# Kernel optimization log

Measured on AMD Instinct MI355X. Metric: run time of the kernel, lower is better.

## Reference

```python
import jax, jax.numpy as jnp
import numpy as np

S, T, B = 128, 64, 64          # src_len, trg_len, batch
E, H, D, A, V = 512, 512, 1024, 256, 32000  # emb, enc_hid, dec_hid(=2H), attn, vocab
PAD = 0


def _p(key, shape, scale=0.02):
    return jax.random.normal(key, shape, dtype=jnp.float32) * scale


def setup_inputs() -> dict:
    key = jax.random.key(0)
    ks = jax.random.split(key, 20)
    return {
        'src': jax.random.randint(ks[0], (S, B), 0, V, dtype=jnp.int32),
        'trg': jax.random.randint(ks[1], (T, B), 0, V, dtype=jnp.int32),
        'enc_emb': _p(ks[2], (V, E)),
        'Wf_ih': _p(ks[3], (4 * H, E)), 'Wf_hh': _p(ks[4], (4 * H, H)), 'bf': jnp.zeros((4 * H,), jnp.float32),
        'Wb_ih': _p(ks[5], (4 * H, E)), 'Wb_hh': _p(ks[6], (4 * H, H)), 'bb': jnp.zeros((4 * H,), jnp.float32),
        'Wa': _p(ks[7], (A, 2 * H + D)), 'ba': jnp.zeros((A,), jnp.float32),
        'v': _p(ks[8], (A,)),
        'dec_emb': _p(ks[9], (V, E)),
        'Wd_ih': _p(ks[10], (4 * D, E + 2 * H)), 'Wd_hh': _p(ks[11], (4 * D, D)), 'bd': jnp.zeros((4 * D,), jnp.float32),
        'Wo': _p(ks[12], (V, 2 * H + D + E)), 'bo': jnp.zeros((V,), jnp.float32),
    }


def lstm_cell(x, h, c, W_ih, W_hh, b):
    # PyTorch gate order: i, f, g, o
    g = x @ W_ih.T + h @ W_hh.T + b
    i, f, gg, o = jnp.split(g, 4, axis=-1)
    c2 = jax.nn.sigmoid(f) * c + jax.nn.sigmoid(i) * jnp.tanh(gg)
    h2 = jax.nn.sigmoid(o) * jnp.tanh(c2)
    return h2, c2


def seq2seq_fwd(src, trg, enc_emb, Wf_ih, Wf_hh, bf, Wb_ih, Wb_hh, bb,
                Wa, ba, v, dec_emb, Wd_ih, Wd_hh, bd, Wo, bo):
    emb = enc_emb[src]                                   # [S,B,E]
    z = jnp.zeros((B, H), emb.dtype)

    def fstep(carry, x):
        h, c = lstm_cell(x, *carry, Wf_ih, Wf_hh, bf)
        return (h, c), h

    def bstep(carry, x):
        h, c = lstm_cell(x, *carry, Wb_ih, Wb_hh, bb)
        return (h, c), h

    (hf, cf), hs_f = jax.lax.scan(fstep, (z, z), emb)
    (hb, cb), hs_b = jax.lax.scan(bstep, (z, z), emb[::-1])
    enc_out = jnp.concatenate([hs_f, hs_b[::-1]], axis=-1)   # [S,B,2H]

    h0 = jnp.concatenate([hf, hb], axis=-1)              # [B,D]
    c0 = jnp.concatenate([cf, cb], axis=-1)

    mask = (src != PAD).T                                # [B,S]
    enc_bse = enc_out.transpose(1, 0, 2)                 # [B,S,2H]

    def dstep(carry, tok):
        h, c = carry
        emb_t = dec_emb[tok]                             # [B,E]
        hrep = jnp.broadcast_to(h[:, None, :], (B, S, D))
        energy = jnp.tanh(jnp.concatenate([hrep, enc_bse], -1) @ Wa.T + ba)  # [B,S,A]
        scores = energy @ v                              # [B,S]
        scores = jnp.where(mask, scores, jnp.float32(-1e10))
        a = jax.nn.softmax(scores, axis=1)
        ctx = jnp.einsum('bs,bse->be', a, enc_bse)       # [B,2H]
        x = jnp.concatenate([emb_t, ctx], axis=-1)
        h2, c2 = lstm_cell(x, h, c, Wd_ih, Wd_hh, bd)
        pred = jnp.concatenate([h2, ctx, emb_t], -1) @ Wo.T + bo  # [B,V]
        return (h2, c2), pred

    # teacher_forcing_ratio = 1.0 -> input at step t is trg[t-1]
    _, preds = jax.lax.scan(dstep, (h0, c0), trg[:-1])
    outputs = jnp.concatenate([jnp.zeros((1, B, V), preds.dtype), preds], axis=0)
    return outputs                                       # [T,B,V]


def reference(src, trg, enc_emb, Wf_ih, Wf_hh, bf, Wb_ih, Wb_hh, bb,
              Wa, ba, v, dec_emb, Wd_ih, Wd_hh, bd, Wo, bo):
    return seq2seq_fwd(src, trg, enc_emb, Wf_ih, Wf_hh, bf, Wb_ih, Wb_hh, bb,
                       Wa, ba, v, dec_emb, Wd_ih, Wd_hh, bd, Wo, bo)
```

## Files before the change

kernel.cpp:

```cpp
#include <hip/hip_runtime.h>

#define SLEN  128
#define BATCH 64
#define EMB   512
#define HID   512
#define DDEC  1024
#define ATT   256
#define VOC   32000
#define TSTEPS 63
#define SLOT  1024

typedef _Float16 f16x4 __attribute__((ext_vector_type(4)));
typedef _Float16 f16x8 __attribute__((ext_vector_type(8)));
typedef float    f32x4 __attribute__((ext_vector_type(4)));

union HQ  { unsigned long long q[2]; f16x8 v; };
union HP  { _Float16 h[2]; unsigned u; };
union HP4 { _Float16 h[4]; f16x4 v4; unsigned long long u; };

__device__ __forceinline__ float sigmoidf_(float x) { return 1.0f / (1.0f + __expf(-x)); }
__device__ __forceinline__ float tanhf_(float x)    { return 1.0f - 2.0f / (__expf(2.0f * x) + 1.0f); }

__device__ __forceinline__ void st_u32(void* p, unsigned v) {
    __hip_atomic_store((unsigned*)p, v, __ATOMIC_RELAXED, __HIP_MEMORY_SCOPE_AGENT);
}
__device__ __forceinline__ void st_u64(void* p, unsigned long long v) {
    __hip_atomic_store((unsigned long long*)p, v, __ATOMIC_RELAXED, __HIP_MEMORY_SCOPE_AGENT);
}
__device__ __forceinline__ unsigned long long ld_u64(const void* p) {
    return __hip_atomic_load((const unsigned long long*)p, __ATOMIC_RELAXED, __HIP_MEMORY_SCOPE_AGENT);
}
__device__ __forceinline__ void st_i32(int* p, int v) {
    __hip_atomic_store(p, v, __ATOMIC_RELAXED, __HIP_MEMORY_SCOPE_AGENT);
}
__device__ __forceinline__ int ld_i32(const int* p) {
    return __hip_atomic_load(p, __ATOMIC_RELAXED, __HIP_MEMORY_SCOPE_AGENT);
}

__device__ __forceinline__ void bar_arrive(int* flags, int myid, int epoch) {
    __syncthreads();
    if (threadIdx.x == 0) st_i32(flags + myid * SLOT, epoch);
}
__device__ __forceinline__ void bar_wait(int* flags, int nf, int epoch) {
    if ((int)threadIdx.x < 64) {
        bool done = false;
        while (!done) {
            bool ok = true;
            for (int i = threadIdx.x; i < nf; i += 64)
                ok = ok && (ld_i32(flags + i * SLOT) >= epoch);
            done = __all(ok);
            if (!done) __builtin_amdgcn_s_sleep(1);
        }
    }
    __syncthreads();
}

__global__ __launch_bounds__(256) void init_convert(
    const int* __restrict__ src, const int* __restrict__ trg,
    const float* __restrict__ enc_emb, const float* __restrict__ dec_emb,
    const float* __restrict__ Wf_ih, const float* __restrict__ Wf_hh,
    const float* __restrict__ Wb_ih, const float* __restrict__ Wb_hh,
    const float* __restrict__ Wa, const float* __restrict__ Wd_ih, const float* __restrict__ Wd_hh,
    float* __restrict__ out0,
    _Float16* __restrict__ Wenc16, _Float16* __restrict__ Wd16, _Float16* __restrict__ Wa16,
    _Float16* __restrict__ emb_src16, _Float16* __restrict__ predA,
    float* __restrict__ c_enc, _Float16* __restrict__ h16_enc, int* __restrict__ bar_ws)
{
    long idx = (long)blockIdx.x * 256 + threadIdx.x;
    if (idx < 2048000L) { out0[idx] = 0.f; return; }
    idx -= 2048000L;
    if (idx < 4194304L) {
        int dir = (int)(idx >> 21);
        int rem = (int)(idx & ((1 << 21) - 1));
        int rr = rem >> 10, c = rem & 1023;
        int d = rr >> 2, qg = rr & 3;
        const float* Wih = dir ? Wb_ih : Wf_ih;
        const float* Whh = dir ? Wb_hh : Wf_hh;
        float v = (c < 512) ? Wih[(long)(qg * 512 + d) * 512 + c]
                            : Whh[(long)(qg * 512 + d) * 512 + (c - 512)];
        Wenc16[idx] = (_Float16)v; return;
    }
    idx -= 4194304L;
    if (idx < 10485760L) {
        int rr = (int)(idx / 2560), c = (int)(idx % 2560);
        int d = rr >> 2, qg = rr & 3;
        float v = (c < 1536) ? Wd_ih[(long)(qg * 1024 + d) * 1536 + c]
                             : Wd_hh[(long)(qg * 1024 + d) * 1024 + (c - 1536)];
        Wd16[idx] = (_Float16)v; return;
    }
    idx -= 10485760L;
    if (idx < 262144L) {
        int rr = (int)(idx >> 10), c = (int)(idx & 1023);
        Wa16[idx] = (_Float16)Wa[(long)rr * 2048 + c]; return;
    }
    idx -= 262144L;
    if (idx < 4194304L) {
        int sb = (int)(idx >> 9), e = (int)(idx & 511);
        int tok = src[sb];
        emb_src16[idx] = (_Float16)enc_emb[(long)tok * 512 + e]; return;
    }
    idx -= 4194304L;
    if (idx < 2064384L) {
        int rI = (int)(idx >> 9), e = (int)(idx & 511);
        int tok = trg[rI];
        predA[(long)(64 + rI) * 2560 + 2048 + e] = (_Float16)dec_emb[(long)tok * 512 + e]; return;
    }
    idx -= 2064384L;
    if (idx < 65536L) { c_enc[idx] = 0.f; return; }
    idx -= 65536L;
    if (idx < 65536L) { h16_enc[idx] = (_Float16)0.f; return; }
    idx -= 65536L;
    if (idx < 655360L) { bar_ws[idx] = 0; }
}

__global__ __launch_bounds__(256, 1) void enc_coop(
    const _Float16* __restrict__ Wenc16, const _Float16* __restrict__ emb_src16,
    _Float16* __restrict__ h16_enc, float* __restrict__ c_enc,
    const float* __restrict__ bf, const float* __restrict__ bb,
    _Float16* __restrict__ enc_out16, int* __restrict__ bar_ws)
{
    __shared__ _Float16 Wl[32768];
    __shared__ float gbuf[32][34];

    const int t = threadIdx.x, lane = t & 63, wv = t >> 6;
    const int blk = blockIdx.x;
    const int g = blk >> 6, wb = blk & 63;
    const int dir = g >> 1, bh = g & 1;
    const int r16 = lane & 15, kg = lane >> 4;
    int* eflags = bar_ws + (384 + g * 64) * SLOT;

    #pragma unroll
    for (int i = 0; i < 16; ++i) {
        int h0 = (i * 256 + t) * 8;
        int kc = h0 >> 10;
        int rem = h0 & 1023;
        int gt2 = rem >> 9, l = (rem >> 3) & 63;
        f16x8 v = *(const f16x8*)(Wenc16 +
            ((size_t)(dir * 2048 + wb * 32 + gt2 * 16 + (l & 15))) * 1024 + (l >> 4) * 8 + kc * 32);
        *(f16x8*)&Wl[h0] = v;
    }

    const float* bias = dir ? bb : bf;
    const int pb = t & 31, dp = t >> 5;
    const int dl0 = dp * 2;
    float bias2[2][4], creg2[2] = {0.f, 0.f};
    if (t < 128) {
        #pragma unroll
        for (int j = 0; j < 2; ++j)
            #pragma unroll
            for (int q = 0; q < 4; ++q)
                bias2[j][q] = bias[q * 512 + wb * 8 + dl0 + j];
    }
    __syncthreads();

    for (int s = 0; s < SLEN; ++s) {
        const int par = s & 1;
        const int s_eff = dir ? (127 - s) : s;
        const int gt = wv & 1, mb = wv >> 1;
        const int arow = bh * 32 + mb * 16 + r16;
        const _Float16* Ax = emb_src16 + ((size_t)(s_eff * 64 + arow)) * 512 + kg * 8;
        const unsigned long long* Hq =
            (const unsigned long long*)(h16_enc + ((size_t)((par * 2 + dir) * 64 + arow)) * 512);
        f32x4 acc = {};
        #pragma unroll 4
        for (int kc = 0; kc < 16; ++kc) {
            f16x8 bw = *(const f16x8*)&Wl[kc * 1024 + gt * 512 + lane * 8];
            f16x8 a  = *(const f16x8*)(Ax + kc * 32);
            acc = __builtin_amdgcn_mfma_f32_16x16x32_f16(a, bw, acc, 0, 0, 0);
        }
        #pragma unroll 4
        for (int kc = 0; kc < 16; ++kc) {
            f16x8 bw = *(const f16x8*)&Wl[(16 + kc) * 1024 + gt * 512 + lane * 8];
            HQ hq;
            hq.q[0] = ld_u64(Hq + kc * 8 + kg * 2);
            hq.q[1] = ld_u64(Hq + kc * 8 + kg * 2 + 1);
            acc = __builtin_amdgcn_mfma_f32_16x16x32_f16(hq.v, bw, acc, 0, 0, 0);
        }
        #pragma unroll
        for (int rI = 0; rI < 4; ++rI)
            gbuf[gt * 16 + (lane & 15)][mb * 16 + kg * 4 + rI] = acc[rI];
        __syncthreads();
        if (t < 128) {
            HP hp;
            #pragma unroll
            for (int j = 0; j < 2; ++j) {
                const int dl = dl0 + j;
                float g0 = gbuf[dl * 4 + 0][pb] + bias2[j][0];
                float g1 = gbuf[dl * 4 + 1][pb] + bias2[j][1];
                float g2 = gbuf[dl * 4 + 2][pb] + bias2[j][2];
                float g3 = gbuf[dl * 4 + 3][pb] + bias2[j][3];
                float c2 = sigmoidf_(g1) * creg2[j] + sigmoidf_(g0) * tanhf_(g2);
                float h2 = sigmoidf_(g3) * tanhf_(c2);
                creg2[j] = c2;
                hp.h[j] = (_Float16)h2;
            }
            const int bglob = bh * 32 + pb;
            const int d0 = wb * 8 + dl0;
            st_u32((void*)(h16_enc + ((size_t)((par ^ 1) * 2 + dir) * 64 + bglob) * 512 + d0), hp.u);
            *(unsigned*)(enc_out16 + ((size_t)s_eff * 64 + bglob) * 1024 + dir * 512 + d0) = hp.u;
        }
        bar_arrive(eflags, wb, s + 1);
        bar_wait(eflags, 64, s + 1);
    }
    if (t < 128) {
        const int bglob = bh * 32 + pb;
        const int d0 = wb * 8 + dl0;
        c_enc[((size_t)dir * 64 + bglob) * 512 + d0] = creg2[0];
        c_enc[((size_t)dir * 64 + bglob) * 512 + d0 + 1] = creg2[1];
    }
}

__global__ __launch_bounds__(256, 1) void dec_coop(
    const _Float16* __restrict__ Wd16, const _Float16* __restrict__ Wa16,
    const float* __restrict__ bd, const float* __restrict__ vvec,
    const int* __restrict__ src, const _Float16* __restrict__ enc_part16,
    const _Float16* __restrict__ enc_out16, const float* __restrict__ c_enc,
    _Float16* __restrict__ predA, int* __restrict__ bar_ws)
{
    __shared__ _Float16 Wl[40960];
    __shared__ float gbuf[16][68];
    __shared__ float ha[256], sv[256], sc[128], esum[256], red[4];

    const int t = threadIdx.x, lane = t & 63, wv = t >> 6;
    const int r16 = lane & 15, kg = lane >> 4;
    const int blk = blockIdx.x;
    const int gid = blk;
    int* cf  = bar_ws;
    int* hs  = bar_ws + 64 * SLOT;
    int* hf0 = bar_ws + 320 * SLOT;

    #pragma unroll
    for (int i = 0; i < 20; ++i) {
        int h0 = (i * 256 + t) * 8;
        int kc = h0 >> 9, l = (h0 >> 3) & 63;
        f16x8 v = *(const f16x8*)(Wd16 + ((size_t)(gid * 16 + (l & 15))) * 2560 + (l >> 4) * 8 + kc * 32);
        *(f16x8*)&Wl[h0] = v;
    }

    const int pb = t & 63;
    const int dl0 = (t >> 6) * 2;
    float bias2[2][4], creg2[2] = {0.f, 0.f};
    if (t < 128) {
        #pragma unroll
        for (int j = 0; j < 2; ++j) {
            const int dg = gid * 4 + dl0 + j;
            #pragma unroll
            for (int q = 0; q < 4; ++q) bias2[j][q] = bd[q * 1024 + dg];
            creg2[j] = (dg < 512) ? c_enc[(size_t)pb * 512 + dg]
                                  : c_enc[(size_t)(64 + pb) * 512 + (dg - 512)];
        }
    }

    if (blk < 64) {
        sv[t] = vvec[t];
        {
            const int d0 = t * 4;
            const size_t rbase = (d0 < 512) ? (size_t)(127 * 64 + blk) * 1024
                                            : (size_t)(0 * 64 + blk) * 1024;
            HP4 o;
            o.h[0] = enc_out16[rbase + d0];
            o.h[1] = enc_out16[rbase + d0 + 1];
            o.h[2] = enc_out16[rbase + d0 + 2];
            o.h[3] = enc_out16[rbase + d0 + 3];
            st_u64((void*)(predA + (size_t)blk * 2560 + d0), o.u);
        }
        bar_arrive(hf0, blk, 1);
    } else {
        __syncthreads();
    }

    for (int tt = 0; tt < TSTEPS; ++tt) {
        if (tt == 0) bar_wait(hf0, 64, 1); else bar_wait(hs, 256, tt);

        if (blk < 64) {
            const int wb = blk;
            {
                const int base_m = wb & 48;
                const _Float16* Ahh = predA + ((size_t)(tt * 64 + base_m + r16)) * 2560 + kg * 8;
                f32x4 acc4[4] = {};
                #pragma unroll 4
                for (int kc = 0; kc < 32; ++kc) {
                    f16x8 a = *(const f16x8*)(Ahh + kc * 32);
                    #pragma unroll
                    for (int jj = 0; jj < 4; ++jj) {
                        f16x8 bw = *(const f16x8*)(Wa16 +
                            ((size_t)((wv * 4 + jj) * 16 + r16)) * 1024 + kg * 8 + kc * 32);
                        acc4[jj] = __builtin_amdgcn_mfma_f32_16x16x32_f16(a, bw, acc4[jj], 0, 0, 0);
                    }
                }
                if (kg == ((wb & 15) >> 2)) {
                    #pragma unroll
                    for (int jj = 0; jj < 4; ++jj)
                        ha[(wv * 4 + jj) * 16 + r16] = acc4[jj][wb & 3];
                }
            }
            __syncthreads();
            {
                const int s = t & 127, jh = t >> 7;
                const f16x8* ep = (const f16x8*)(enc_part16 + ((size_t)s * 64 + wb) * 256 + jh * 128);
                float acc = 0.f;
                #pragma unroll 2
                for (int j8 = 0; j8 < 16; ++j8) {
                    f16x8 e = ep[j8];
                    #pragma unroll
                    for (int u = 0; u < 8; ++u)
                        acc += tanhf_(ha[jh * 128 + j8 * 8 + u] + (float)e[u]) * sv[jh * 128 + j8 * 8 + u];
                }
                esum[t] = acc;
            }
            __syncthreads();
            if (t < 128) {
                float scv = esum[t] + esum[128 + t];
                scv = (src[t * 64 + wb] != 0) ? scv : -1e10f;
                sc[t] = scv;
                float v = scv;
                #pragma unroll
                for (int off = 32; off > 0; off >>= 1) v = fmaxf(v, __shfl_xor(v, off));
                if (lane == 0) red[t >> 6] = v;
            }
            __syncthreads();
            {
                const float mx = fmaxf(red[0], red[1]);
                if (t < 128) {
                    float e = __expf(sc[t] - mx);
                    sc[t] = e;
                    float v = e;
                    #pragma unroll
                    for (int off = 32; off > 0; off >>= 1) v += __shfl_xor(v, off);
                    if (lane == 0) red[2 + (t >> 6)] = v;
                }
            }
            __syncthreads();
            {
                const float inv = 1.0f / (red[2] + red[3]);
                float a0 = 0.f, a1 = 0.f, a2 = 0.f, a3 = 0.f;
                #pragma unroll 4
                for (int sI = 0; sI < 128; ++sI) {
                    float as = sc[sI] * inv;
                    f16x4 ev = *(const f16x4*)(enc_out16 + ((size_t)sI * 64 + wb) * 1024 + t * 4);
                    a0 += as * (float)ev[0]; a1 += as * (float)ev[1];
                    a2 += as * (float)ev[2]; a3 += as * (float)ev[3];
                }
                HP4 o;
                o.h[0] = (_Float16)a0; o.h[1] = (_Float16)a1;
                o.h[2] = (_Float16)a2; o.h[3] = (_Float16)a3;
                st_u64((void*)(predA + ((size_t)(64 + tt * 64 + wb)) * 2560 + 1024 + t * 4), o.u);
            }
            bar_arrive(cf, wb, tt + 1);
        }

        {
            const int mb = wv;
            const _Float16* Ae = predA + ((size_t)(64 + tt * 64 + mb * 16 + r16)) * 2560 + kg * 8;
            const _Float16* Ah = predA + ((size_t)(tt * 64 + mb * 16 + r16)) * 2560 + kg * 8;
            f32x4 acc = {};
            #pragma unroll 4
            for (int kc = 0; kc < 16; ++kc) {
                f16x8 bw = *(const f16x8*)&Wl[kc * 512 + lane * 8];
                f16x8 a  = *(const f16x8*)(Ae + 2048 + kc * 32);
                acc = __builtin_amdgcn_mfma_f32_16x16x32_f16(a, bw, acc, 0, 0, 0);
            }
            #pragma unroll 4
            for (int kc = 0; kc < 32; ++kc) {
                f16x8 bw = *(const f16x8*)&Wl[(48 + kc) * 512 + lane * 8];
                f16x8 a  = *(const f16x8*)(Ah + kc * 32);
                acc = __builtin_amdgcn_mfma_f32_16x16x32_f16(a, bw, acc, 0, 0, 0);
            }
            bar_wait(cf, 64, tt + 1);
            #pragma unroll 4
            for (int kc = 0; kc < 32; ++kc) {
                f16x8 bw = *(const f16x8*)&Wl[(16 + kc) * 512 + lane * 8];
                f16x8 a  = *(const f16x8*)(Ae + 1024 + kc * 32);
                acc = __builtin_amdgcn_mfma_f32_16x16x32_f16(a, bw, acc, 0, 0, 0);
            }
            #pragma unroll
            for (int rI = 0; rI < 4; ++rI)
                gbuf[lane & 15][mb * 16 + kg * 4 + rI] = acc[rI];
        }
        __syncthreads();
        if (t < 128) {
            HP hp;
            #pragma unroll
            for (int j = 0; j < 2; ++j) {
                const int dl = dl0 + j;
                float g0 = gbuf[dl * 4 + 0][pb] + bias2[j][0];
                float g1 = gbuf[dl * 4 + 1][pb] + bias2[j][1];
                float g2 = gbuf[dl * 4 + 2][pb] + bias2[j][2];
                float g3 = gbuf[dl * 4 + 3][pb] + bias2[j][3];
                float c2 = sigmoidf_(g1) * creg2[j] + sigmoidf_(g0) * tanhf_(g2);
                float h2 = sigmoidf_(g3) * tanhf_(c2);
                creg2[j] = c2;
                hp.h[j] = (_Float16)h2;
            }
            st_u32((void*)(predA + ((size_t)(64 + tt * 64 + pb)) * 2560 + gid * 4 + dl0), hp.u);
        }
        bar_arrive(hs, gid, tt + 1);
    }
}

__global__ __launch_bounds__(64) void enc_step_mfma(
    const _Float16* __restrict__ Wenc16, const _Float16* __restrict__ emb_src16,
    _Float16* __restrict__ h16_enc, float* __restrict__ c_enc,
    const float* __restrict__ bf, const float* __restrict__ bb,
    _Float16* __restrict__ enc_out16, int s)
{
    __shared__ float gbuf[16 * 66];
    const int lane = threadIdx.x;
    const int blk = blockIdx.x;
    const int dir = blk >> 7, tile = blk & 127;
    const int par = s & 1;
    const int s_eff = dir ? (SLEN - 1 - s) : s;
    const int r16 = lane & 15, kg = lane >> 4;

    const _Float16* Bw = Wenc16 + ((size_t)(dir * 2048 + tile * 16 + r16)) * 1024 + kg * 8;
    const _Float16* Ax = emb_src16 + ((size_t)(s_eff * 64 + r16)) * 512 + kg * 8;
    const _Float16* Ah = h16_enc + ((size_t)((par * 2 + dir) * 64 + r16)) * 512 + kg * 8;

    f32x4 acc[4] = {};
    #pragma unroll 4
    for (int kc = 0; kc < 16; ++kc) {
        f16x8 bfr = *(const f16x8*)(Bw + kc * 32);
        #pragma unroll
        for (int m = 0; m < 4; ++m) {
            f16x8 a = *(const f16x8*)(Ax + kc * 32 + (size_t)m * 16 * 512);
            acc[m] = __builtin_amdgcn_mfma_f32_16x16x32_f16(a, bfr, acc[m], 0, 0, 0);
        }
    }
    #pragma unroll 4
    for (int kc = 0; kc < 16; ++kc) {
        f16x8 bfr = *(const f16x8*)(Bw + 512 + kc * 32);
        #pragma unroll
        for (int m = 0; m < 4; ++m) {
            f16x8 a = *(const f16x8*)(Ah + kc * 32 + (size_t)m * 16 * 512);
            acc[m] = __builtin_amdgcn_mfma_f32_16x16x32_f16(a, bfr, acc[m], 0, 0, 0);
        }
    }
    #pragma unroll
    for (int m = 0; m < 4; ++m)
        #pragma unroll
        for (int rI = 0; rI < 4; ++rI)
            gbuf[r16 * 66 + m * 16 + kg * 4 + rI] = acc[m][rI];
    __syncthreads();

    const float* bias = dir ? bb : bf;
    const int b = lane;
    #pragma unroll
    for (int dl = 0; dl < 4; ++dl) {
        const int d = tile * 4 + dl;
        float g0 = gbuf[(dl * 4 + 0) * 66 + b] + bias[d];
        float g1 = gbuf[(dl * 4 + 1) * 66 + b] + bias[512 + d];
        float g2 = gbuf[(dl * 4 + 2) * 66 + b] + bias[1024 + d];
        float g3 = gbuf[(dl * 4 + 3) * 66 + b] + bias[1536 + d];
        const size_t cur = ((size_t)(par * 2 + dir) * 64 + b) * 512 + d;
        const size_t nxt = ((size_t)((par ^ 1) * 2 + dir) * 64 + b) * 512 + d;
        float c2 = sigmoidf_(g1) * c_enc[cur] + sigmoidf_(g0) * tanhf_(g2);
        float h2 = sigmoidf_(g3) * tanhf_(c2);
        c_enc[nxt] = c2;
        h16_enc[nxt] = (_Float16)h2;
        enc_out16[((size_t)s_eff * 64 + b) * 1024 + dir * 512 + d] = (_Float16)h2;
    }
}

__global__ __launch_bounds__(256) void dec_init(
    const _Float16* __restrict__ enc_out16, const float* __restrict__ c_enc,
    _Float16* __restrict__ predA, float* __restrict__ c_dec)
{
    int idx = blockIdx.x * 256 + threadIdx.x;
    int b = (idx >> 10) & 63, d = idx & 1023;
    if (idx < 65536) {
        _Float16 v = (d < 512) ? enc_out16[(size_t)(127 * 64 + b) * 1024 + d]
                               : enc_out16[(size_t)(0 * 64 + b) * 1024 + d];
        predA[(size_t)b * 2560 + d] = v;
    } else {
        float v = (d < 512) ? c_enc[((size_t)(0 * 2 + 0) * 64 + b) * 512 + d]
                            : c_enc[((size_t)(0 * 2 + 1) * 64 + b) * 512 + (d - 512)];
        c_dec[(size_t)b * 1024 + d] = v;
    }
}

__global__ __launch_bounds__(64) void hatt_mfma(
    const _Float16* __restrict__ predA, const _Float16* __restrict__ Wa16,
    float* __restrict__ hatt, int t)
{
    const int lane = threadIdx.x;
    const int tile = blockIdx.x;
    const int r16 = lane & 15, kg = lane >> 4;
    const _Float16* Ap = predA + ((size_t)(t * 64 + r16)) * 2560 + kg * 8;
    const _Float16* Bw = Wa16 + ((size_t)(tile * 16 + r16)) * 1024 + kg * 8;
    f32x4 acc[4] = {};
    #pragma unroll 4
    for (int kc = 0; kc < 32; ++kc) {
        f16x8 bfr = *(const f16x8*)(Bw + kc * 32);
        #pragma unroll
        for (int m = 0; m < 4; ++m) {
            f16x8 a = *(const f16x8*)(Ap + kc * 32 + (size_t)m * 16 * 2560);
            acc[m] = __builtin_amdgcn_mfma_f32_16x16x32_f16(a, bfr, acc[m], 0, 0, 0);
        }
    }
    #pragma unroll
    for (int m = 0; m < 4; ++m)
        #pragma unroll
        for (int rI = 0; rI < 4; ++rI)
            hatt[(size_t)(m * 16 + kg * 4 + rI) * 256 + tile * 16 + r16] = acc[m][rI];
}

__global__ __launch_bounds__(256) void attn_step(
    const int* __restrict__ src, const float* __restrict__ hatt, const float* __restrict__ vvec,
    const _Float16* __restrict__ enc_part16, const _Float16* __restrict__ enc_out16,
    _Float16* __restrict__ predA, int t)
{
    __shared__ float ha[256], sv[256], sc[128], red[128];
    const int b = blockIdx.x, tid = threadIdx.x;
    ha[tid] = hatt[b * 256 + tid];
    sv[tid] = vvec[tid];
    __syncthreads();
    if (tid < 128) {
        const f16x8* ep = (const f16x8*)(enc_part16 + ((size_t)tid * 64 + b) * 256);
        float acc = 0.f;
        #pragma unroll 4
        for (int j8 = 0; j8 < 32; ++j8) {
            f16x8 e = ep[j8];
            #pragma unroll
            for (int u = 0; u < 8; ++u)
                acc += tanhf_(ha[j8 * 8 + u] + (float)e[u]) * sv[j8 * 8 + u];
        }
        float scv = (src[tid * 64 + b] != 0) ? acc : -1e10f;
        sc[tid] = scv; red[tid] = scv;
    }
    __syncthreads();
    for (int off = 64; off > 0; off >>= 1) { if (tid < off) red[tid] = fmaxf(red[tid], red[tid + off]); __syncthreads(); }
    const float mx = red[0];
    __syncthreads();
    if (tid < 128) { float e = __expf(sc[tid] - mx); sc[tid] = e; red[tid] = e; }
    __syncthreads();
    for (int off = 64; off > 0; off >>= 1) { if (tid < off) red[tid] += red[tid + off]; __syncthreads(); }
    const float inv = 1.0f / red[0];
    __syncthreads();

    float a0 = 0.f, a1 = 0.f, a2 = 0.f, a3 = 0.f;
    for (int sI = 0; sI < 128; ++sI) {
        float as = sc[sI] * inv;
        f16x4 ev = *(const f16x4*)(enc_out16 + ((size_t)sI * 64 + b) * 1024 + tid * 4);
        a0 += as * (float)ev[0]; a1 += as * (float)ev[1];
        a2 += as * (float)ev[2]; a3 += as * (float)ev[3];
    }
    f16x4 o = { (_Float16)a0, (_Float16)a1, (_Float16)a2, (_Float16)a3 };
    *(f16x4*)(predA + ((size_t)(64 + t * 64 + b)) * 2560 + 1024 + tid * 4) = o;
}

__global__ __launch_bounds__(64) void dec_gates(
    const _Float16* __restrict__ Wd16, const float* __restrict__ bd,
    float* __restrict__ c_dec, _Float16* __restrict__ predA, int t)
{
    __shared__ float gbuf[16 * 66];
    const int lane = threadIdx.x;
    const int tile = blockIdx.x;
    const int par = t & 1;
    const int r16 = lane & 15, kg = lane >> 4;
    const _Float16* Bw = Wd16 + ((size_t)(tile * 16 + r16)) * 2560 + kg * 8;
    const _Float16* At = predA + ((size_t)(64 + t * 64 + r16)) * 2560 + kg * 8;
    const _Float16* Ah = predA + ((size_t)(t * 64 + r16)) * 2560 + kg * 8;
    f32x4 acc[4] = {};
    #pragma unroll 4
    for (int kc = 0; kc < 16; ++kc) {
        f16x8 bfr = *(const f16x8*)(Bw + kc * 32);
        #pragma unroll
        for (int m = 0; m < 4; ++m) {
            f16x8 a = *(const f16x8*)(At + 2048 + kc * 32 + (size_t)m * 16 * 2560);
            acc[m] = __builtin_amdgcn_mfma_f32_16x16x32_f16(a, bfr, acc[m], 0, 0, 0);
        }
    }
    #pragma unroll 4
    for (int kc = 0; kc < 32; ++kc) {
        f16x8 bfr = *(const f16x8*)(Bw + 512 + kc * 32);
        #pragma unroll
        for (int m = 0; m < 4; ++m) {
            f16x8 a = *(const f16x8*)(At + 1024 + kc * 32 + (size_t)m * 16 * 2560);
            acc[m] = __builtin_amdgcn_mfma_f32_16x16x32_f16(a, bfr, acc[m], 0, 0, 0);
        }
    }
    #pragma unroll 4
    for (int kc = 0; kc < 32; ++kc) {
        f16x8 bfr = *(const f16x8*)(Bw + 1536 + kc * 32);
        #pragma unroll
        for (int m = 0; m < 4; ++m) {
            f16x8 a = *(const f16x8*)(Ah + kc * 32 + (size_t)m * 16 * 2560);
            acc[m] = __builtin_amdgcn_mfma_f32_16x16x32_f16(a, bfr, acc[m], 0, 0, 0);
        }
    }
    #pragma unroll
    for (int m = 0; m < 4; ++m)
        #pragma unroll
        for (int rI = 0; rI < 4; ++rI)
            gbuf[r16 * 66 + m * 16 + kg * 4 + rI] = acc[m][rI];
    __syncthreads();

    const int b = lane;
    #pragma unroll
    for (int dl = 0; dl < 4; ++dl) {
        const int d = tile * 4 + dl;
        float g0 = gbuf[(dl * 4 + 0) * 66 + b] + bd[d];
        float g1 = gbuf[(dl * 4 + 1) * 66 + b] + bd[1024 + d];
        float g2 = gbuf[(dl * 4 + 2) * 66 + b] + bd[2048 + d];
        float g3 = gbuf[(dl * 4 + 3) * 66 + b] + bd[3072 + d];
        float c2 = sigmoidf_(g1) * c_dec[(size_t)(par * 64 + b) * 1024 + d] + sigmoidf_(g0) * tanhf_(g2);
        float h2 = sigmoidf_(g3) * tanhf_(c2);
        c_dec[(size_t)((par ^ 1) * 64 + b) * 1024 + d] = c2;
        predA[((size_t)(64 + t * 64 + b)) * 2560 + d] = (_Float16)h2;
    }
}

__global__ __launch_bounds__(256, 2) void gemm_a16(
    const _Float16* __restrict__ A, int lda,
    const float* __restrict__ B, int ldb,
    const float* __restrict__ bias,
    void* __restrict__ Cv, int ldc, int K, int Mvalid, int ntn, int c16)
{
    __shared__ _Float16 As[8192];
    __shared__ _Float16 Bs[8192];

    const int nwg = gridDim.x;
    const int id = blockIdx.x;
    const int q = nwg >> 3, r = nwg & 7;
    const int xcd = id & 7, ix = id >> 3;
    const int wg = (xcd < r) ? (xcd * (q + 1) + ix) : (r * (q + 1) + (xcd - r) * q + ix);
    const int per = ntn << 3;
    const int g = wg / per, rem = wg % per;
    const int mt = g * 8 + (rem & 7), nt = rem >> 3;

    const int t = threadIdx.x, lane = t & 63, wid = t >> 6;
    const int wr = wid >> 1, wc = wid & 1;

    const int arow_s = t >> 3, ac8 = t & 7;
    const int brow_s = t >> 4, bc4 = t & 15;
    const _Float16* Ap = A + (size_t)(mt * 128 + arow_s) * lda + ac8 * 8;
    const float*    Bp = B + (size_t)(nt * 128 + brow_s) * ldb + bc4 * 4;
    const int awx = (ac8 * 8) ^ ((arow_s & 7) << 3);
    const int bwx = (bc4 * 4) ^ ((brow_s & 7) << 3);

    const int kts = K >> 6;
    f32x4 acc[4][4] = {};
    f16x8 ra[4]; float4 rb[8];
    #pragma unroll
    for (int i = 0; i < 4; ++i) ra[i] = *(const f16x8*)(Ap + (size_t)i * 32 * lda);
    #pragma unroll
    for (int i = 0; i < 8; ++i) rb[i] = *(const float4*)(Bp + (size_t)i * 16 * ldb);

    const int abase = (wr * 64 + (lane & 15)) * 64 + (lane >> 4) * 8;
    const int bbase = (wc * 64 + (lane & 15)) * 64 + (lane >> 4) * 8;
    const int sxor = (lane & 7) << 3;

    for (int kt = 0; kt < kts; ++kt) {
        f16x4 cb[8];
        #pragma unroll
        for (int i = 0; i < 8; ++i)
            cb[i] = (f16x4){(_Float16)rb[i].x, (_Float16)rb[i].y, (_Float16)rb[i].z, (_Float16)rb[i].w};
        __syncthreads();
        #pragma unroll
        for (int i = 0; i < 4; ++i)
            *(f16x8*)&As[(arow_s + i * 32) * 64 + awx] = ra[i];
        #pragma unroll
        for (int i = 0; i < 8; ++i)
            *(f16x4*)&Bs[(brow_s + i * 16) * 64 + bwx] = cb[i];
        __syncthreads();
        if (kt + 1 < kts) {
            #pragma unroll
            for (int i = 0; i < 4; ++i) ra[i] = *(const f16x8*)(Ap + (size_t)i * 32 * lda + (kt + 1) * 64);
            #pragma unroll
            for (int i = 0; i < 8; ++i) rb[i] = *(const float4*)(Bp + (size_t)i * 16 * ldb + (kt + 1) * 64);
        }
        #pragma unroll
        for (int kk = 0; kk < 2; ++kk) {
            f16x8 af[4], bfr[4];
            #pragma unroll
            for (int m = 0; m < 4; ++m) af[m]  = *(const f16x8*)&As[(abase + m * 16 * 64 + kk * 32) ^ sxor];
            #pragma unroll
            for (int n = 0; n < 4; ++n) bfr[n] = *(const f16x8*)&Bs[(bbase + n * 16 * 64 + kk * 32) ^ sxor];
            #pragma unroll
            for (int m = 0; m < 4; ++m)
                #pragma unroll
                for (int n = 0; n < 4; ++n)
                    acc[m][n] = __builtin_amdgcn_mfma_f32_16x16x32_f16(af[m], bfr[n], acc[m][n], 0, 0, 0);
        }
    }

    const int ccol = nt * 128 + wc * 64 + (lane & 15);
    const int crow0 = mt * 128 + wr * 64 + ((lane >> 4) << 2);
    float bv[4];
    #pragma unroll
    for (int n = 0; n < 4; ++n) bv[n] = bias[ccol + n * 16];
    #pragma unroll
    for (int m = 0; m < 4; ++m) {
        #pragma unroll
        for (int rI = 0; rI < 4; ++rI) {
            const int row = crow0 + m * 16 + rI;
            if (row < Mvalid) {
                if (c16) {
                    _Float16* C = (_Float16*)Cv;
                    #pragma unroll
                    for (int n = 0; n < 4; ++n)
                        C[(size_t)row * ldc + ccol + n * 16] = (_Float16)(acc[m][n][rI] + bv[n]);
                } else {
                    float* C = (float*)Cv;
                    #pragma unroll
                    for (int n = 0; n < 4; ++n)
                        C[(size_t)row * ldc + ccol + n * 16] = acc[m][n][rI] + bv[n];
                }
            }
        }
    }
}

extern "C" void kernel_launch(void* const* d_in, const int* in_sizes, int n_in,
                              void* d_out, int out_size, void* d_ws, size_t ws_size,
                              hipStream_t stream) {
    const int*   src     = (const int*)d_in[0];
    const int*   trg     = (const int*)d_in[1];
    const float* enc_emb = (const float*)d_in[2];
    const float* Wf_ih   = (const float*)d_in[3];
    const float* Wf_hh   = (const float*)d_in[4];
    const float* bf      = (const float*)d_in[5];
    const float* Wb_ih   = (const float*)d_in[6];
    const float* Wb_hh   = (const float*)d_in[7];
    const float* bb      = (const float*)d_in[8];
    const float* Wa      = (const float*)d_in[9];
    const float* ba      = (const float*)d_in[10];
    const float* vvec    = (const float*)d_in[11];
    const float* dec_emb = (const float*)d_in[12];
    const float* Wd_ih   = (const float*)d_in[13];
    const float* Wd_hh   = (const float*)d_in[14];
    const float* bd      = (const float*)d_in[15];
    const float* Wo      = (const float*)d_in[16];
    const float* bo      = (const float*)d_in[17];
    float* out = (float*)d_out;

    char* w = (char*)d_ws;
    _Float16* Wenc16     = (_Float16*)(w);
    _Float16* Wd16       = (_Float16*)(w + 8388608);
    _Float16* Wa16       = (_Float16*)(w + 29360128);
    _Float16* emb_src16  = (_Float16*)(w + 29884416);
    _Float16* enc_out16  = (_Float16*)(w + 38273024);
    _Float16* predA      = (_Float16*)(w + 55050240);
    _Float16* h16_enc    = (_Float16*)(w + 76349440);
    float*    c_enc      = (float*)   (w + 76611584);
    float*    c_dec      = (float*)   (w + 77135872);
    float*    hatt       = (float*)   (w + 77660160);
    _Float16* enc_part16 = (_Float16*)(w + 77725696);
    int*      bar_ws     = (int*)     (w + 81920000);
    const size_t need_bytes = 84541440;
    if (ws_size < need_bytes) return;

    init_convert<<<93888, 256, 0, stream>>>(
        src, trg, enc_emb, dec_emb, Wf_ih, Wf_hh, Wb_ih, Wb_hh, Wa, Wd_ih, Wd_hh,
        out, Wenc16, Wd16, Wa16, emb_src16, predA, c_enc, h16_enc, bar_ws);

    {
        const _Float16* a0 = Wenc16; const _Float16* a1 = emb_src16;
        _Float16* a2 = h16_enc; float* a3 = c_enc;
        const float* a4 = bf; const float* a5 = bb;
        _Float16* a6 = enc_out16; int* a7 = bar_ws;
        void* args[] = { &a0, &a1, &a2, &a3, &a4, &a5, &a6, &a7 };
        hipError_t e = hipLaunchCooperativeKernel((const void*)enc_coop, dim3(256), dim3(256), args, 0, stream);
        if (e != hipSuccess) {
            for (int s = 0; s < SLEN; ++s)
                enc_step_mfma<<<256, 64, 0, stream>>>(Wenc16, emb_src16, h16_enc, c_enc, bf, bb, enc_out16, s);
        }
    }

    gemm_a16<<<128, 256, 0, stream>>>(enc_out16, 1024, Wa + 1024, 2048, ba,
                                      enc_part16, 256, 1024, 8192, 2, 1);

    {
        const _Float16* a0 = Wd16; const _Float16* a1 = Wa16;
        const float* a2 = bd; const float* a3 = vvec;
        const int* a4 = src; const _Float16* a5 = enc_part16;
        const _Float16* a6 = enc_out16; const float* a7 = c_enc;
        _Float16* a8 = predA; int* a9 = bar_ws;
        void* args[] = { &a0, &a1, &a2, &a3, &a4, &a5, &a6, &a7, &a8, &a9 };
        hipError_t e = hipLaunchCooperativeKernel((const void*)dec_coop, dim3(256), dim3(256), args, 0, stream);
        if (e != hipSuccess) {
            dec_init<<<512, 256, 0, stream>>>(enc_out16, c_enc, predA, c_dec);
            for (int t = 0; t < TSTEPS; ++t) {
                hatt_mfma<<<16, 64, 0, stream>>>(predA, Wa16, hatt, t);
                attn_step<<<64, 256, 0, stream>>>(src, hatt, vvec, enc_part16, enc_out16, predA, t);
                dec_gates<<<256, 64, 0, stream>>>(Wd16, bd, c_dec, predA, t);
            }
        }
    }

    gemm_a16<<<8000, 256, 0, stream>>>(predA + (size_t)64 * 2560, 2560, Wo, 2560, bo,
                                       out + (size_t)64 * VOC, VOC, 2560, 4032, 250, 0);
}
```

Baseline: 5.116 ms.

## Rebalance decoder LSTM rows away from attention blocks and batch operand loads

The cooperative decoder kernel now splits gate rows unevenly. The 64 attention blocks each own 1 hidden unit, and the other 192 blocks each own 5 units, computed with two MFMA accumulators. This shortens the per-step critical path through the attention blocks. The encoder and attention GEMMs now load their A-operands into register arrays before the MFMA chains, and the context reduction uses 8-wide loads split across two halves of the source sequence. Shared memory is repacked into one buffer with aliased regions. The costs are higher register pressure and padded MFMA work in the 5-unit blocks.

```diff
diff --git a/kernel.cpp b/kernel.cpp
--- a/kernel.cpp
+++ b/kernel.cpp
@@ -17,6 +17,7 @@
 union HQ  { unsigned long long q[2]; f16x8 v; };
 union HP  { _Float16 h[2]; unsigned u; };
 union HP4 { _Float16 h[4]; f16x4 v4; unsigned long long u; };
+union HPs { _Float16 h; unsigned short u; };
 
 __device__ __forceinline__ float sigmoidf_(float x) { return 1.0f / (1.0f + __expf(-x)); }
 __device__ __forceinline__ float tanhf_(float x)    { return 1.0f - 2.0f / (__expf(2.0f * x) + 1.0f); }
@@ -26,6 +27,9 @@
 }
 __device__ __forceinline__ void st_u64(void* p, unsigned long long v) {
     __hip_atomic_store((unsigned long long*)p, v, __ATOMIC_RELAXED, __HIP_MEMORY_SCOPE_AGENT);
+}
+__device__ __forceinline__ void st_u16(void* p, unsigned short v) {
+    __hip_atomic_store((unsigned short*)p, v, __ATOMIC_RELAXED, __HIP_MEMORY_SCOPE_AGENT);
 }
 __device__ __forceinline__ unsigned long long ld_u64(const void* p) {
     return __hip_atomic_load((const unsigned long long*)p, __ATOMIC_RELAXED, __HIP_MEMORY_SCOPE_AGENT);
@@ -162,19 +166,26 @@
         const unsigned long long* Hq =
             (const unsigned long long*)(h16_enc + ((size_t)((par * 2 + dir) * 64 + arow)) * 512);
         f32x4 acc = {};
-        #pragma unroll 4
-        for (int kc = 0; kc < 16; ++kc) {
-            f16x8 bw = *(const f16x8*)&Wl[kc * 1024 + gt * 512 + lane * 8];
-            f16x8 a  = *(const f16x8*)(Ax + kc * 32);
-            acc = __builtin_amdgcn_mfma_f32_16x16x32_f16(a, bw, acc, 0, 0, 0);
-        }
-        #pragma unroll 4
-        for (int kc = 0; kc < 16; ++kc) {
-            f16x8 bw = *(const f16x8*)&Wl[(16 + kc) * 1024 + gt * 512 + lane * 8];
-            HQ hq;
-            hq.q[0] = ld_u64(Hq + kc * 8 + kg * 2);
-            hq.q[1] = ld_u64(Hq + kc * 8 + kg * 2 + 1);
-            acc = __builtin_amdgcn_mfma_f32_16x16x32_f16(hq.v, bw, acc, 0, 0, 0);
+        {
+            f16x8 aX[16];
+            #pragma unroll
+            for (int kc = 0; kc < 16; ++kc) aX[kc] = *(const f16x8*)(Ax + kc * 32);
+            #pragma unroll
+            for (int kc = 0; kc < 16; ++kc) {
+                f16x8 bw = *(const f16x8*)&Wl[kc * 1024 + gt * 512 + lane * 8];
+                acc = __builtin_amdgcn_mfma_f32_16x16x32_f16(aX[kc], bw, acc, 0, 0, 0);
+            }
+            HQ hq[16];
+            #pragma unroll
+            for (int kc = 0; kc < 16; ++kc) {
+                hq[kc].q[0] = ld_u64(Hq + kc * 8 + kg * 2);
+                hq[kc].q[1] = ld_u64(Hq + kc * 8 + kg * 2 + 1);
+            }
+            #pragma unroll
+            for (int kc = 0; kc < 16; ++kc) {
+                f16x8 bw = *(const f16x8*)&Wl[(16 + kc) * 1024 + gt * 512 + lane * 8];
+                acc = __builtin_amdgcn_mfma_f32_16x16x32_f16(hq[kc].v, bw, acc, 0, 0, 0);
+            }
         }
         #pragma unroll
         for (int rI = 0; rI < 4; ++rI)
@@ -217,53 +228,70 @@
     const _Float16* __restrict__ enc_out16, const float* __restrict__ c_enc,
     _Float16* __restrict__ predA, int* __restrict__ bar_ws)
 {
-    __shared__ _Float16 Wl[40960];
-    __shared__ float gbuf[16][68];
-    __shared__ float ha[256], sv[256], sc[128], esum[256], red[4];
+    __shared__ char smem[110592];
+    _Float16* Wl = (_Float16*)smem;
+    float (*gbuf)[66] = (float(*)[66])(smem + 102400);
+    float* ha   = (float*)(smem + 20480);
+    float* sv   = (float*)(smem + 21504);
+    float* sc   = (float*)(smem + 22528);
+    float* red  = (float*)(smem + 23040);
+    float* ectx = (float*)(smem + 24576);
 
     const int t = threadIdx.x, lane = t & 63, wv = t >> 6;
     const int r16 = lane & 15, kg = lane >> 4;
     const int blk = blockIdx.x;
-    const int gid = blk;
+    const bool isAttn = blk < 64;
+    const int nd = isAttn ? 1 : 5;
+    const int nr = nd * 4;
+    const int dbase = isAttn ? blk : (64 + (blk - 64) * 5);
+    const int rowbase = dbase * 4;
     int* cf  = bar_ws;
     int* hs  = bar_ws + 64 * SLOT;
     int* hf0 = bar_ws + 320 * SLOT;
 
-    #pragma unroll
-    for (int i = 0; i < 20; ++i) {
-        int h0 = (i * 256 + t) * 8;
-        int kc = h0 >> 9, l = (h0 >> 3) & 63;
-        f16x8 v = *(const f16x8*)(Wd16 + ((size_t)(gid * 16 + (l & 15))) * 2560 + (l >> 4) * 8 + kc * 32);
-        *(f16x8*)&Wl[h0] = v;
-    }
-
-    const int pb = t & 63;
-    const int dl0 = (t >> 6) * 2;
-    float bias2[2][4], creg2[2] = {0.f, 0.f};
-    if (t < 128) {
-        #pragma unroll
-        for (int j = 0; j < 2; ++j) {
-            const int dg = gid * 4 + dl0 + j;
-            #pragma unroll
-            for (int q = 0; q < 4; ++q) bias2[j][q] = bd[q * 1024 + dg];
-            creg2[j] = (dg < 512) ? c_enc[(size_t)pb * 512 + dg]
-                                  : c_enc[(size_t)(64 + pb) * 512 + (dg - 512)];
-        }
-    }
-
-    if (blk < 64) {
+    {
+        const int nfrag = nr * 320;
+        for (int f = t; f < nfrag; f += 256) {
+            int kc = f / (nr * 4);
+            int rem = f - kc * (nr * 4);
+            int r = rem >> 2, kq = rem & 3;
+            *(f16x8*)&Wl[((kc * nr + r) << 5) + kq * 8] =
+                *(const f16x8*)(Wd16 + (size_t)(rowbase + r) * 2560 + kc * 32 + kq * 8);
+        }
+    }
+
+    float creg[2] = {0.f, 0.f};
+    float biasA[2][4];
+    int pdk[2] = {0, 0}, pbk[2] = {0, 0};
+    bool pvalid[2] = {false, false};
+    #pragma unroll
+    for (int k = 0; k < 2; ++k) {
+        int p = t + k * 256;
+        if (p < nd * 64) {
+            pvalid[k] = true;
+            pdk[k] = p >> 6; pbk[k] = p & 63;
+            int dg = dbase + pdk[k];
+            #pragma unroll
+            for (int q = 0; q < 4; ++q) biasA[k][q] = bd[q * 1024 + dg];
+            creg[k] = (dg < 512) ? c_enc[(size_t)pbk[k] * 512 + dg]
+                                 : c_enc[(size_t)(64 + pbk[k]) * 512 + (dg - 512)];
+        }
+    }
+
+    const int rc0 = (r16 < nr) ? r16 : (nr - 1);
+    const int rc1 = (16 + r16 < nr) ? (16 + r16) : (nr - 1);
+
+    if (isAttn) {
         sv[t] = vvec[t];
-        {
-            const int d0 = t * 4;
-            const size_t rbase = (d0 < 512) ? (size_t)(127 * 64 + blk) * 1024
-                                            : (size_t)(0 * 64 + blk) * 1024;
-            HP4 o;
-            o.h[0] = enc_out16[rbase + d0];
-            o.h[1] = enc_out16[rbase + d0 + 1];
-            o.h[2] = enc_out16[rbase + d0 + 2];
-            o.h[3] = enc_out16[rbase + d0 + 3];
-            st_u64((void*)(predA + (size_t)blk * 2560 + d0), o.u);
-        }
+        const int d0 = t * 4;
+        const size_t rbase = (d0 < 512) ? (size_t)(127 * 64 + blk) * 1024
+                                        : (size_t)(0 * 64 + blk) * 1024;
+        HP4 o;
+        o.h[0] = enc_out16[rbase + d0];
+        o.h[1] = enc_out16[rbase + d0 + 1];
+        o.h[2] = enc_out16[rbase + d0 + 2];
+        o.h[3] = enc_out16[rbase + d0 + 3];
+        st_u64((void*)(predA + (size_t)blk * 2560 + d0), o.u);
         bar_arrive(hf0, blk, 1);
     } else {
         __syncthreads();
@@ -272,20 +300,22 @@
     for (int tt = 0; tt < TSTEPS; ++tt) {
         if (tt == 0) bar_wait(hf0, 64, 1); else bar_wait(hs, 256, tt);
 
-        if (blk < 64) {
+        if (isAttn) {
             const int wb = blk;
             {
                 const int base_m = wb & 48;
                 const _Float16* Ahh = predA + ((size_t)(tt * 64 + base_m + r16)) * 2560 + kg * 8;
+                f16x8 aP[32];
+                #pragma unroll
+                for (int kc = 0; kc < 32; ++kc) aP[kc] = *(const f16x8*)(Ahh + kc * 32);
                 f32x4 acc4[4] = {};
-                #pragma unroll 4
+                #pragma unroll
                 for (int kc = 0; kc < 32; ++kc) {
-                    f16x8 a = *(const f16x8*)(Ahh + kc * 32);
                     #pragma unroll
                     for (int jj = 0; jj < 4; ++jj) {
                         f16x8 bw = *(const f16x8*)(Wa16 +
                             ((size_t)((wv * 4 + jj) * 16 + r16)) * 1024 + kg * 8 + kc * 32);
-                        acc4[jj] = __builtin_amdgcn_mfma_f32_16x16x32_f16(a, bw, acc4[jj], 0, 0, 0);
+                        acc4[jj] = __builtin_amdgcn_mfma_f32_16x16x32_f16(aP[kc], bw, acc4[jj], 0, 0, 0);
                     }
                 }
                 if (kg == ((wb & 15) >> 2)) {
@@ -299,18 +329,18 @@
                 const int s = t & 127, jh = t >> 7;
                 const f16x8* ep = (const f16x8*)(enc_part16 + ((size_t)s * 64 + wb) * 256 + jh * 128);
                 float acc = 0.f;
-                #pragma unroll 2
+                #pragma unroll
                 for (int j8 = 0; j8 < 16; ++j8) {
                     f16x8 e = ep[j8];
                     #pragma unroll
                     for (int u = 0; u < 8; ++u)
                         acc += tanhf_(ha[jh * 128 + j8 * 8 + u] + (float)e[u]) * sv[jh * 128 + j8 * 8 + u];
                 }
-                esum[t] = acc;
+                ectx[t] = acc;
             }
             __syncthreads();
             if (t < 128) {
-                float scv = esum[t] + esum[128 + t];
+                float scv = ectx[t] + ectx[128 + t];
                 scv = (src[t * 64 + wb] != 0) ? scv : -1e10f;
                 sc[t] = scv;
                 float v = scv;
@@ -333,18 +363,29 @@
             __syncthreads();
             {
                 const float inv = 1.0f / (red[2] + red[3]);
-                float a0 = 0.f, a1 = 0.f, a2 = 0.f, a3 = 0.f;
-                #pragma unroll 4
-                for (int sI = 0; sI < 128; ++sI) {
-                    float as = sc[sI] * inv;
-                    f16x4 ev = *(const f16x4*)(enc_out16 + ((size_t)sI * 64 + wb) * 1024 + t * 4);
-                    a0 += as * (float)ev[0]; a1 += as * (float)ev[1];
-                    a2 += as * (float)ev[2]; a3 += as * (float)ev[3];
+                const int eg = t & 127, sh = t >> 7;
+                float a[8] = {0.f, 0.f, 0.f, 0.f, 0.f, 0.f, 0.f, 0.f};
+                #pragma unroll 8
+                for (int i = 0; i < 64; ++i) {
+                    const int sI = sh * 64 + i;
+                    const float as = sc[sI] * inv;
+                    f16x8 ev = *(const f16x8*)(enc_out16 + ((size_t)sI * 64 + wb) * 1024 + eg * 8);
+                    #pragma unroll
+                    for (int u = 0; u < 8; ++u) a[u] += as * (float)ev[u];
                 }
-                HP4 o;
-                o.h[0] = (_Float16)a0; o.h[1] = (_Float16)a1;
-                o.h[2] = (_Float16)a2; o.h[3] = (_Float16)a3;
-                st_u64((void*)(predA + ((size_t)(64 + tt * 64 + wb)) * 2560 + 1024 + t * 4), o.u);
+                #pragma unroll
+                for (int u = 0; u < 8; ++u) ectx[t * 8 + u] = a[u];
+            }
+            __syncthreads();
+            if (t < 128) {
+                HP4 o1, o2;
+                #pragma unroll
+                for (int u = 0; u < 4; ++u) {
+                    o1.h[u] = (_Float16)(ectx[t * 8 + u] + ectx[(128 + t) * 8 + u]);
+                    o2.h[u] = (_Float16)(ectx[t * 8 + 4 + u] + ectx[(128 + t) * 8 + 4 + u]);
+                }
+                st_u64((void*)(predA + ((size_t)(64 + tt * 64 + wb)) * 2560 + 1024 + t * 8), o1.u);
+                st_u64((void*)(predA + ((size_t)(64 + tt * 64 + wb)) * 2560 + 1024 + t * 8 + 4), o2.u);
             }
             bar_arrive(cf, wb, tt + 1);
         }
@@ -352,49 +393,79 @@
         {
             const int mb = wv;
             const _Float16* Ae = predA + ((size_t)(64 + tt * 64 + mb * 16 + r16)) * 2560 + kg * 8;
-            const _Float16* Ah = predA + ((size_t)(tt * 64 + mb * 16 + r16)) * 2560 + kg * 8;
-            f32x4 acc = {};
-            #pragma unroll 4
+            const _Float16* Ahp = predA + ((size_t)(tt * 64 + mb * 16 + r16)) * 2560 + kg * 8;
+            f32x4 acc0 = {}, acc1 = {};
+            f16x8 aR[16];
+            #pragma unroll
+            for (int kc = 0; kc < 16; ++kc) aR[kc] = *(const f16x8*)(Ae + 2048 + kc * 32);
+            #pragma unroll
             for (int kc = 0; kc < 16; ++kc) {
-                f16x8 bw = *(const f16x8*)&Wl[kc * 512 + lane * 8];
-                f16x8 a  = *(const f16x8*)(Ae + 2048 + kc * 32);
-                acc = __builtin_amdgcn_mfma_f32_16x16x32_f16(a, bw, acc, 0, 0, 0);
-            }
-            #pragma unroll 4
-            for (int kc = 0; kc < 32; ++kc) {
-                f16x8 bw = *(const f16x8*)&Wl[(48 + kc) * 512 + lane * 8];
-                f16x8 a  = *(const f16x8*)(Ah + kc * 32);
-                acc = __builtin_amdgcn_mfma_f32_16x16x32_f16(a, bw, acc, 0, 0, 0);
+                acc0 = __builtin_amdgcn_mfma_f32_16x16x32_f16(aR[kc], *(const f16x8*)&Wl[((kc * nr + rc0) << 5) + kg * 8], acc0, 0, 0, 0);
+                if (!isAttn)
+                    acc1 = __builtin_amdgcn_mfma_f32_16x16x32_f16(aR[kc], *(const f16x8*)&Wl[((kc * nr + rc1) << 5) + kg * 8], acc1, 0, 0, 0);
+            }
+            #pragma unroll
+            for (int kc = 0; kc < 16; ++kc) aR[kc] = *(const f16x8*)(Ahp + kc * 32);
+            #pragma unroll
+            for (int kc = 0; kc < 16; ++kc) {
+                acc0 = __builtin_amdgcn_mfma_f32_16x16x32_f16(aR[kc], *(const f16x8*)&Wl[(((48 + kc) * nr + rc0) << 5) + kg * 8], acc0, 0, 0, 0);
+                if (!isAttn)
+                    acc1 = __builtin_amdgcn_mfma_f32_16x16x32_f16(aR[kc], *(const f16x8*)&Wl[(((48 + kc) * nr + rc1) << 5) + kg * 8], acc1, 0, 0, 0);
+            }
+            #pragma unroll
+            for (int kc = 0; kc < 16; ++kc) aR[kc] = *(const f16x8*)(Ahp + 512 + kc * 32);
+            #pragma unroll
+            for (int kc = 0; kc < 16; ++kc) {
+                acc0 = __builtin_amdgcn_mfma_f32_16x16x32_f16(aR[kc], *(const f16x8*)&Wl[(((64 + kc) * nr + rc0) << 5) + kg * 8], acc0, 0, 0, 0);
+                if (!isAttn)
+                    acc1 = __builtin_amdgcn_mfma_f32_16x16x32_f16(aR[kc], *(const f16x8*)&Wl[(((64 + kc) * nr + rc1) << 5) + kg * 8], acc1, 0, 0, 0);
             }
             bar_wait(cf, 64, tt + 1);
-            #pragma unroll 4
-            for (int kc = 0; kc < 32; ++kc) {
-                f16x8 bw = *(const f16x8*)&Wl[(16 + kc) * 512 + lane * 8];
-                f16x8 a  = *(const f16x8*)(Ae + 1024 + kc * 32);
-                acc = __builtin_amdgcn_mfma_f32_16x16x32_f16(a, bw, acc, 0, 0, 0);
-            }
-            #pragma unroll
-            for (int rI = 0; rI < 4; ++rI)
-                gbuf[lane & 15][mb * 16 + kg * 4 + rI] = acc[rI];
+            #pragma unroll
+            for (int kc = 0; kc < 16; ++kc) aR[kc] = *(const f16x8*)(Ae + 1024 + kc * 32);
+            #pragma unroll
+            for (int kc = 0; kc < 16; ++kc) {
+                acc0 = __builtin_amdgcn_mfma_f32_16x16x32_f16(aR[kc], *(const f16x8*)&Wl[(((16 + kc) * nr + rc0) << 5) + kg * 8], acc0, 0, 0, 0);
+                if (!isAttn)
+                    acc1 = __builtin_amdgcn_mfma_f32_16x16x32_f16(aR[kc], *(const f16x8*)&Wl[(((16 + kc) * nr + rc1) << 5) + kg * 8], acc1, 0, 0, 0);
+            }
+            #pragma unroll
+            for (int kc = 0; kc < 16; ++kc) aR[kc] = *(const f16x8*)(Ae + 1536 + kc * 32);
+            #pragma unroll
+            for (int kc = 0; kc < 16; ++kc) {
+                acc0 = __builtin_amdgcn_mfma_f32_16x16x32_f16(aR[kc], *(const f16x8*)&Wl[(((32 + kc) * nr + rc0) << 5) + kg * 8], acc0, 0, 0, 0);
+                if (!isAttn)
+                    acc1 = __builtin_amdgcn_mfma_f32_16x16x32_f16(aR[kc], *(const f16x8*)&Wl[(((32 + kc) * nr + rc1) << 5) + kg * 8], acc1, 0, 0, 0);
+            }
+            const int nc0 = lane & 15;
+            if (nc0 < nr) {
+                #pragma unroll
+                for (int rI = 0; rI < 4; ++rI)
+                    gbuf[nc0][mb * 16 + kg * 4 + rI] = acc0[rI];
+            }
+            const int nc1 = 16 + (lane & 15);
+            if (!isAttn && nc1 < nr) {
+                #pragma unroll
+                for (int rI = 0; rI < 4; ++rI)
+                    gbuf[nc1][mb * 16 + kg * 4 + rI] = acc1[rI];
+            }
         }
         __syncthreads();
-        if (t < 128) {
-            HP hp;
-            #pragma unroll
-            for (int j = 0; j < 2; ++j) {
-                const int dl = dl0 + j;
-                float g0 = gbuf[dl * 4 + 0][pb] + bias2[j][0];
-                float g1 = gbuf[dl * 4 + 1][pb] + bias2[j][1];
-                float g2 = gbuf[dl * 4 + 2][pb] + bias2[j][2];
-                float g3 = gbuf[dl * 4 + 3][pb] + bias2[j][3];
-                float c2 = sigmoidf_(g1) * creg2[j] + sigmoidf_(g0) * tanhf_(g2);
+        #pragma unroll
+        for (int k = 0; k < 2; ++k) {
+            if (pvalid[k]) {
+                float g0 = gbuf[pdk[k] * 4 + 0][pbk[k]] + biasA[k][0];
+                float g1 = gbuf[pdk[k] * 4 + 1][pbk[k]] + biasA[k][1];
+                float g2 = gbuf[pdk[k] * 4 + 2][pbk[k]] + biasA[k][2];
+                float g3 = gbuf[pdk[k] * 4 + 3][pbk[k]] + biasA[k][3];
+                float c2 = sigmoidf_(g1) * creg[k] + sigmoidf_(g0) * tanhf_(g2);
                 float h2 = sigmoidf_(g3) * tanhf_(c2);
-                creg2[j] = c2;
-                hp.h[j] = (_Float16)h2;
-            }
-            st_u32((void*)(predA + ((size_t)(64 + tt * 64 + pb)) * 2560 + gid * 4 + dl0), hp.u);
-        }
-        bar_arrive(hs, gid, tt + 1);
+                creg[k] = c2;
+                HPs hp; hp.h = (_Float16)h2;
+                st_u16((void*)(predA + ((size_t)(64 + tt * 64 + pbk[k])) * 2560 + dbase + pdk[k]), hp.u);
+            }
+        }
+        bar_arrive(hs, blk, tt + 1);
     }
 }
 
```

Result: slower. 5.351 ms (+4.6%).
